# Performance work log

Measured on AMD Instinct MI355X. Metric: run time of the kernel, lower is better.

## Reference

```python
import jax, jax.numpy as jnp
import numpy as np

NUM_HEADS = 8
EMBED_DIM = 512
MAX_SEQ = 2048
HEAD_DIM = EMBED_DIM // NUM_HEADS
B, S = 2, 2048


def setup_inputs() -> dict:
    key = jax.random.key(0)
    ks = jax.random.split(key, 12)
    sd = 1.0 / np.sqrt(EMBED_DIM)
    return {
        "q_in": jax.random.normal(ks[0], (B, S, EMBED_DIM), jnp.float32),
        "k_in": jax.random.normal(ks[1], (B, S, EMBED_DIM), jnp.float32),
        "v_in": jax.random.normal(ks[2], (B, S, EMBED_DIM), jnp.float32),
        "Wq": jax.random.normal(ks[3], (EMBED_DIM, EMBED_DIM), jnp.float32) * sd,
        "bq": jnp.zeros((EMBED_DIM,), jnp.float32),
        "Wk": jax.random.normal(ks[4], (EMBED_DIM, EMBED_DIM), jnp.float32) * sd,
        "bk": jnp.zeros((EMBED_DIM,), jnp.float32),
        "Wv": jax.random.normal(ks[5], (EMBED_DIM, EMBED_DIM), jnp.float32) * sd,
        "bv": jnp.zeros((EMBED_DIM,), jnp.float32),
        "Wo": jax.random.normal(ks[6], (EMBED_DIM, EMBED_DIM), jnp.float32) * sd,
        "bo": jnp.zeros((EMBED_DIM,), jnp.float32),
        "rel_emb": jax.random.normal(ks[7], (MAX_SEQ, HEAD_DIM), jnp.float32) * sd,
    }


def _split_heads(x, W, b):
    # x: [B,S,E] -> [B,H,S,D]
    y = x @ W + b
    b_, s_ = y.shape[0], y.shape[1]
    return y.reshape(b_, s_, NUM_HEADS, HEAD_DIM).transpose(0, 2, 1, 3)


def _relative_scores(q, rel_emb):
    # q: [B,H,L,D]; rel_emb sliced to last L rows: [M,D] with M == L here
    L = q.shape[2]
    rel = rel_emb[max(0, MAX_SEQ - L):, :]
    M = rel.shape[0]
    scores = jnp.einsum('bhld,md->bhlm', q, rel)
    # mask = flip(tri(L,M), axis=-1): zero out future relative positions
    mask = jnp.flip(jnp.tri(L, M, dtype=jnp.float32), axis=1)
    scores = scores * mask
    # skew trick: pad one column on the left, reshape swapping last two dims, drop first row
    padded = jnp.pad(scores, ((0, 0), (0, 0), (0, 0), (1, 0)))  # [B,H,L,M+1]
    reshaped = padded.reshape(padded.shape[0], padded.shape[1], M + 1, L)
    skewed = reshaped[:, :, 1:, :]  # [B,H,M,L] == [B,H,L,L]
    return skewed


def reference(q_in, k_in, v_in, Wq, bq, Wk, bk, Wv, bv, Wo, bo, rel_emb):
    q = _split_heads(q_in, Wq, bq)  # [B,H,S,D]
    k = _split_heads(k_in, Wk, bk)
    v = _split_heads(v_in, Wv, bv)
    scores = jnp.einsum('bhqd,bhkd->bhqk', q, k)
    rel_scores = _relative_scores(q, rel_emb)
    logits = (scores + rel_scores) / jnp.sqrt(jnp.float32(HEAD_DIM))
    attn = jax.nn.softmax(logits, axis=-1)
    out = jnp.einsum('bhqk,bhkd->bhqd', attn, v)  # [B,H,S,D]
    merged = out.transpose(0, 2, 1, 3).reshape(out.shape[0], -1, EMBED_DIM)
    return merged @ Wo + bo, attn
```

## Files before the change

kernel.cpp:

```cpp
#include <hip/hip_runtime.h>


typedef __attribute__((ext_vector_type(4))) float f32x4;
typedef __attribute__((ext_vector_type(8))) short short8;

__device__ inline unsigned short f2bf(float x) {
    unsigned u = __float_as_uint(x);
    unsigned r = (u + 0x7fffu + ((u >> 16) & 1u)) >> 16;
    return (unsigned short)r;
}
__device__ inline float bf2f(unsigned short h) {
    return __uint_as_float(((unsigned)h) << 16);
}
__device__ inline int swz(int row, int bytecol) {
    return (row << 7) + (bytecol ^ ((row & 7) << 4));
}
__device__ inline void cvt4(float4 v, uint2& hi, uint2& lo) {
    unsigned short h0 = f2bf(v.x), h1 = f2bf(v.y), h2 = f2bf(v.z), h3 = f2bf(v.w);
    hi = make_uint2(((unsigned)h1 << 16) | h0, ((unsigned)h3 << 16) | h2);
    lo = make_uint2(((unsigned)f2bf(v.y - bf2f(h1)) << 16) | f2bf(v.x - bf2f(h0)),
                    ((unsigned)f2bf(v.w - bf2f(h3)) << 16) | f2bf(v.z - bf2f(h2)));
}
__device__ inline uint2 cvt4hi(float4 v) {
    return make_uint2(((unsigned)f2bf(v.y) << 16) | f2bf(v.x),
                      ((unsigned)f2bf(v.w) << 16) | f2bf(v.z));
}

__global__ __launch_bounds__(256) void wt_prep4(const float* __restrict__ W0,
                                                const float* __restrict__ W1,
                                                const float* __restrict__ W2,
                                                const float* __restrict__ W3,
                                                unsigned short* __restrict__ wt)
{
    __shared__ float Ls[32][33];
    const int t = threadIdx.x;
    const int z = blockIdx.z;
    const float* W = (z == 0) ? W0 : (z == 1) ? W1 : (z == 2) ? W2 : W3;
    unsigned short* WTh = wt + (size_t)(2 * z) * 262144;
    unsigned short* WTl = wt + (size_t)(2 * z + 1) * 262144;
    const int k0 = blockIdx.x << 5, n0 = blockIdx.y << 5;
#pragma unroll
    for (int i = 0; i < 4; ++i) {
        int idx = (i << 8) + t;
        int kk = idx >> 5, nn = idx & 31;
        Ls[kk][nn] = W[(size_t)(k0 + kk) * 512 + n0 + nn];
    }
    __syncthreads();
#pragma unroll
    for (int i = 0; i < 2; ++i) {
        int idx = (i << 8) + t;
        int nn = idx >> 4, kp = idx & 15;
        float f0 = Ls[2 * kp][nn], f1 = Ls[2 * kp + 1][nn];
        unsigned short h0 = f2bf(f0), h1 = f2bf(f1);
        size_t off = (size_t)(n0 + nn) * 512 + k0 + 2 * kp;
        *(unsigned*)&WTh[off] = ((unsigned)h1 << 16) | h0;
        *(unsigned*)&WTl[off] = ((unsigned)f2bf(f1 - bf2f(h1)) << 16) | f2bf(f0 - bf2f(h0));
    }
}

__global__ __launch_bounds__(256) void rel_prep(const float* __restrict__ rel,
                                                unsigned short* __restrict__ relh)
{
    int idx = (blockIdx.x * 256 + threadIdx.x) << 3;
    float4 a = *(const float4*)&rel[idx];
    float4 b = *(const float4*)&rel[idx + 4];
    uint4 o;
    o.x = ((unsigned)f2bf(a.y) << 16) | f2bf(a.x);
    o.y = ((unsigned)f2bf(a.w) << 16) | f2bf(a.z);
    o.z = ((unsigned)f2bf(b.y) << 16) | f2bf(b.x);
    o.w = ((unsigned)f2bf(b.w) << 16) | f2bf(b.z);
    *(uint4*)&relh[idx] = o;
}

__device__ __forceinline__ void gemm64_core(const float* __restrict__ A,
                                            const unsigned short* __restrict__ WTh,
                                            const unsigned short* __restrict__ WTl,
                                            int m0, int n0, char* smem, int t,
                                            f32x4 (&acc)[4])
{
    char* aH = smem;
    char* aL = smem + 8192;
    char* wH = smem + 16384;
    char* wL = smem + 24576;
    const int lane = t & 63, w = t >> 6;
    const int lr = lane & 15, kg = lane >> 4;

    for (int k0 = 0; k0 < 512; k0 += 64) {
        if (k0) __syncthreads();
#pragma unroll
        for (int i = 0; i < 4; ++i) {
            int idx = (i << 8) + t;
            int row = idx >> 4, c4 = idx & 15;
            float4 v = *(const float4*)&A[(size_t)(m0 + row) * 512 + k0 + (c4 << 2)];
            uint2 hi, lo; cvt4(v, hi, lo);
            int ph = swz(row, c4 << 3);
            *(uint2*)(aH + ph) = hi;
            *(uint2*)(aL + ph) = lo;
        }
#pragma unroll
        for (int i = 0; i < 4; ++i) {
            int idx = (i << 8) + t;
            int plane = idx >> 9, rem = idx & 511;
            int nn = rem >> 3, j8 = rem & 7;
            const unsigned short* src = plane ? WTl : WTh;
            uint4 vv = *(const uint4*)&src[(size_t)(n0 + nn) * 512 + k0 + (j8 << 3)];
            *(uint4*)((plane ? wL : wH) + swz(nn, j8 << 4)) = vv;
        }
        __syncthreads();
#pragma unroll
        for (int kk = 0; kk < 2; ++kk) {
            int bc = (kk << 6) + (kg << 4);
            int ar = (w << 4) + lr;
            short8 a_h = *(const short8*)(aH + swz(ar, bc));
            short8 a_l = *(const short8*)(aL + swz(ar, bc));
#pragma unroll
            for (int f = 0; f < 4; ++f) {
                short8 b_h = *(const short8*)(wH + swz((f << 4) + lr, bc));
                short8 b_l = *(const short8*)(wL + swz((f << 4) + lr, bc));
                acc[f] = __builtin_amdgcn_mfma_f32_16x16x32_bf16(a_h, b_h, acc[f], 0, 0, 0);
                acc[f] = __builtin_amdgcn_mfma_f32_16x16x32_bf16(a_l, b_h, acc[f], 0, 0, 0);
                acc[f] = __builtin_amdgcn_mfma_f32_16x16x32_bf16(a_h, b_l, acc[f], 0, 0, 0);
            }
        }
    }
}

__global__ __launch_bounds__(256) void gemm_qkv(
    const float* __restrict__ Aq, const float* __restrict__ Ak, const float* __restrict__ Av,
    const unsigned short* __restrict__ wt,
    const float* __restrict__ bq, const float* __restrict__ bk, const float* __restrict__ bv,
    unsigned short* __restrict__ qh, unsigned short* __restrict__ ql,
    unsigned short* __restrict__ kh, unsigned short* __restrict__ kl,
    unsigned short* __restrict__ vh, unsigned short* __restrict__ vl)
{
    __shared__ char smem[32768];
    const int t = threadIdx.x;
    const int z = blockIdx.z;
    const int n0 = blockIdx.x << 6;
    const int m0 = blockIdx.y << 6;
    const int lane = t & 63, w = t >> 6;
    const int lr = lane & 15, kg = lane >> 4;

    const float* A = (z == 0) ? Aq : (z == 1) ? Ak : Av;
    const float* bias = (z == 0) ? bq : (z == 1) ? bk : bv;
    const unsigned short* WTh = wt + (size_t)(2 * z) * 262144;
    const unsigned short* WTl = wt + (size_t)(2 * z + 1) * 262144;
    unsigned short* outH = (z == 0) ? qh : (z == 1) ? kh : vh;
    unsigned short* outL = (z == 0) ? ql : (z == 1) ? kl : vl;

    f32x4 acc[4];
#pragma unroll
    for (int f = 0; f < 4; ++f) acc[f] = {0.f, 0.f, 0.f, 0.f};

    gemm64_core(A, WTh, WTl, m0, n0, smem, t, acc);

    const int mbase = m0 + (w << 4) + (kg << 2);
    const int b = mbase >> 11, s = mbase & 2047;
    const int bidx = (b << 3) + (n0 >> 6);
#pragma unroll
    for (int f = 0; f < 4; ++f) {
        int d = (f << 4) + lr;
        float bv_ = bias[n0 + d];
        if (z < 2) {
#pragma unroll
            for (int e = 0; e < 4; ++e) {
                float val = acc[f][e] + bv_;
                unsigned short hh = f2bf(val);
                size_t off = ((size_t)bidx * 2048 + s + e) * 64 + d;
                outH[off] = hh;
                outL[off] = f2bf(val - bf2f(hh));
            }
        } else {
            unsigned short h[4], l[4];
#pragma unroll
            for (int e = 0; e < 4; ++e) {
                float val = acc[f][e] + bv_;
                h[e] = f2bf(val);
                l[e] = f2bf(val - bf2f(h[e]));
            }
            size_t off = ((size_t)bidx * 64 + d) * 2048 + s;
            *(uint2*)&outH[off] = make_uint2(((unsigned)h[1] << 16) | h[0],
                                             ((unsigned)h[3] << 16) | h[2]);
            *(uint2*)&outL[off] = make_uint2(((unsigned)l[1] << 16) | l[0],
                                             ((unsigned)l[3] << 16) | l[2]);
        }
    }
}

__global__ __launch_bounds__(256) void gemm_out(
    const float* __restrict__ pO,
    const unsigned short* __restrict__ WTh, const unsigned short* __restrict__ WTl,
    const float* __restrict__ bias, float* __restrict__ out0)
{
    __shared__ char smem[32768];
    char* aH = smem;
    char* aL = smem + 8192;
    char* wH = smem + 16384;
    char* wL = smem + 24576;
    const int t = threadIdx.x;
    const int n0 = blockIdx.x << 6;
    const int m0 = blockIdx.y << 6;
    const int lane = t & 63, w = t >> 6;
    const int lr = lane & 15, kg = lane >> 4;
    const int bq = m0 >> 11, s0 = m0 & 2047;

    f32x4 acc[4];
#pragma unroll
    for (int f = 0; f < 4; ++f) acc[f] = {0.f, 0.f, 0.f, 0.f};

    for (int k0 = 0; k0 < 512; k0 += 64) {
        if (k0) __syncthreads();
        const float* p0 = pO + ((size_t)((bq << 3) + (k0 >> 6)) * 2048 + s0) * 64;
#pragma unroll
        for (int i = 0; i < 2; ++i) {
            int idx = (i << 8) + t;
            int row = idx >> 3, j8 = idx & 7;
            size_t off = (size_t)row * 64 + (j8 << 3);
            float4 a0 = *(const float4*)&p0[off];
            float4 a1 = *(const float4*)&p0[off + 4];
            float4 b0 = *(const float4*)&p0[off + 2097152];
            float4 b1 = *(const float4*)&p0[off + 4 + 2097152];
            float4 v0 = make_float4(a0.x + b0.x, a0.y + b0.y, a0.z + b0.z, a0.w + b0.w);
            float4 v1 = make_float4(a1.x + b1.x, a1.y + b1.y, a1.z + b1.z, a1.w + b1.w);
            uint2 h0, l0, h1, l1;
            cvt4(v0, h0, l0);
            cvt4(v1, h1, l1);
            int ph = swz(row, j8 << 4);
            *(uint4*)(aH + ph) = make_uint4(h0.x, h0.y, h1.x, h1.y);
            *(uint4*)(aL + ph) = make_uint4(l0.x, l0.y, l1.x, l1.y);
        }
#pragma unroll
        for (int i = 0; i < 4; ++i) {
            int idx = (i << 8) + t;
            int plane = idx >> 9, rem = idx & 511;
            int nn = rem >> 3, j8 = rem & 7;
            const unsigned short* src = plane ? WTl : WTh;
            uint4 vv = *(const uint4*)&src[(size_t)(n0 + nn) * 512 + k0 + (j8 << 3)];
            *(uint4*)((plane ? wL : wH) + swz(nn, j8 << 4)) = vv;
        }
        __syncthreads();
#pragma unroll
        for (int kk = 0; kk < 2; ++kk) {
            int bc = (kk << 6) + (kg << 4);
            int ar = (w << 4) + lr;
            short8 a_h = *(const short8*)(aH + swz(ar, bc));
            short8 a_l = *(const short8*)(aL + swz(ar, bc));
#pragma unroll
            for (int f = 0; f < 4; ++f) {
                short8 b_h = *(const short8*)(wH + swz((f << 4) + lr, bc));
                short8 b_l = *(const short8*)(wL + swz((f << 4) + lr, bc));
                acc[f] = __builtin_amdgcn_mfma_f32_16x16x32_bf16(a_h, b_h, acc[f], 0, 0, 0);
                acc[f] = __builtin_amdgcn_mfma_f32_16x16x32_bf16(a_l, b_h, acc[f], 0, 0, 0);
                acc[f] = __builtin_amdgcn_mfma_f32_16x16x32_bf16(a_h, b_l, acc[f], 0, 0, 0);
            }
        }
    }

    const int mbase = m0 + (w << 4) + (kg << 2);
#pragma unroll
    for (int f = 0; f < 4; ++f) {
        int n = n0 + (f << 4) + lr;
        float bv = bias[n];
#pragma unroll
        for (int e = 0; e < 4; ++e)
            out0[(size_t)(mbase + e) * 512 + n] = acc[f][e] + bv;
    }
}

__global__ __launch_bounds__(512, 4) void logits_flash(
    const unsigned short* __restrict__ qh_g, const unsigned short* __restrict__ ql_g,
    const unsigned short* __restrict__ kh_g, const unsigned short* __restrict__ kl_g,
    const unsigned short* __restrict__ relh_g,
    float* __restrict__ attn, unsigned short* __restrict__ rawh,
    float* __restrict__ tilemax, int mode,
    float2* __restrict__ stats)
{
    __shared__ char smem[59136];
    char* kh = smem;
    char* kl = smem + 16384;
    char* bandP = smem + 32768;
    unsigned short* Pt = (unsigned short*)(smem + 32768);
    float* part_m = (float*)(smem + 58112);
    float* part_z = (float*)(smem + 58624);

    const int t = threadIdx.x;
    const int bh = blockIdx.y;
    int ib = blockIdx.x; if (bh & 8) ib = 31 - ib;
    const int i0 = ib << 6;
    const int lane = t & 63, w = t >> 6;
    const int wr = w >> 1, wc = w & 1;
    const int lr = lane & 15, kg = lane >> 4;
    const int irow = (wr << 4) + lr;

    const size_t qoff = ((size_t)bh * 2048 + i0 + irow) * 64;
    const short8 aH0 = *(const short8*)(qh_g + qoff + (kg << 3));
    const short8 aH1 = *(const short8*)(qh_g + qoff + 32 + (kg << 3));
    const short8 aL0 = *(const short8*)(ql_g + qoff + (kg << 3));
    const short8 aL1 = *(const short8*)(ql_g + qoff + 32 + (kg << 3));

    float rm = -3.0e38f, rz = 0.f;

    const unsigned short* khb = kh_g + (size_t)bh * 2048 * 64;
    const unsigned short* klb = kl_g + (size_t)bh * 2048 * 64;
    const size_t obase = ((size_t)bh * 2048 + i0) * 2048;

    for (int jt = 0; jt < 16; ++jt) {
        const int j0 = jt << 7;
        const bool anyRel = (j0 <= i0 + 63);
        const int m0 = 1984 - i0 + j0;
        __syncthreads();
        if (jt > 0 && t < 64) {
            float m1 = part_m[t], m2 = part_m[64 + t];
            float z1 = part_z[t], z2 = part_z[64 + t];
            float tm = fmaxf(m1, m2);
            float tz = z1 * __expf((m1 - tm) * 0.125f) + z2 * __expf((m2 - tm) * 0.125f);
            float mn = fmaxf(rm, tm);
            rz = rz * __expf((rm - mn) * 0.125f) + tz * __expf((tm - mn) * 0.125f);
            rm = mn;
        }
        {
            int rr = t >> 2, gp = (t & 3) << 1;
            const unsigned short* s0 = khb + (size_t)(j0 + rr) * 64 + (gp << 3);
            *(uint4*)(kh + swz(rr, gp << 4)) = *(const uint4*)s0;
            *(uint4*)(kh + swz(rr, (gp + 1) << 4)) = *(const uint4*)(s0 + 8);
            const unsigned short* s1 = klb + (size_t)(j0 + rr) * 64 + (gp << 3);
            *(uint4*)(kl + swz(rr, gp << 4)) = *(const uint4*)s1;
            *(uint4*)(kl + swz(rr, (gp + 1) << 4)) = *(const uint4*)(s1 + 8);
        }
        if (anyRel) {
#pragma unroll
            for (int i = 0; i < 3; ++i) {
                int idx = (i << 9) + t;
                int row = idx >> 3, g = idx & 7;
                int m = m0 + row; if (m > 2047) m = 2047;
                *(uint4*)(bandP + swz(row, g << 4)) = *(const uint4*)(relh_g + (size_t)m * 64 + (g << 3));
            }
        }
        __syncthreads();

        f32x4 acc[4];
#pragma unroll
        for (int cf = 0; cf < 4; ++cf) {
            int krow = (wc << 6) + (cf << 4) + lr;
            short8 bH0 = *(const short8*)(kh + swz(krow, kg << 4));
            short8 bH1 = *(const short8*)(kh + swz(krow, 64 + (kg << 4)));
            short8 bL0 = *(const short8*)(kl + swz(krow, kg << 4));
            short8 bL1 = *(const short8*)(kl + swz(krow, 64 + (kg << 4)));
            f32x4 c = {0.f, 0.f, 0.f, 0.f};
            c = __builtin_amdgcn_mfma_f32_16x16x32_bf16(bH0, aH0, c, 0, 0, 0);
            c = __builtin_amdgcn_mfma_f32_16x16x32_bf16(bH1, aH1, c, 0, 0, 0);
            c = __builtin_amdgcn_mfma_f32_16x16x32_bf16(bH0, aL0, c, 0, 0, 0);
            c = __builtin_amdgcn_mfma_f32_16x16x32_bf16(bH1, aL1, c, 0, 0, 0);
            c = __builtin_amdgcn_mfma_f32_16x16x32_bf16(bL0, aH0, c, 0, 0, 0);
            c = __builtin_amdgcn_mfma_f32_16x16x32_bf16(bL1, aH1, c, 0, 0, 0);
            acc[cf] = c;
        }
        if (anyRel) {
            f32x4 pr[6];
#pragma unroll
            for (int q = 0; q < 6; ++q) {
                int ff = (wc ? 6 : 0) + q;
                int brow = (ff << 4) + lr;
                short8 rb0 = *(const short8*)(bandP + swz(brow, kg << 4));
                short8 rb1 = *(const short8*)(bandP + swz(brow, 64 + (kg << 4)));
                f32x4 c = {0.f, 0.f, 0.f, 0.f};
                c = __builtin_amdgcn_mfma_f32_16x16x32_bf16(rb0, aH0, c, 0, 0, 0);
                c = __builtin_amdgcn_mfma_f32_16x16x32_bf16(rb1, aH1, c, 0, 0, 0);
                pr[q] = c;
            }
            __syncthreads();
#pragma unroll
            for (int q = 0; q < 6; ++q) {
                int ff = (wc ? 6 : 0) + q;
#pragma unroll
                for (int e = 0; e < 4; ++e)
                    Pt[((ff << 4) + (kg << 2) + e) * 66 + irow] = f2bf(pr[q][e]);
            }
            __syncthreads();
        }

        float rowmax = -3.0e38f;
#pragma unroll
        for (int cf = 0; cf < 4; ++cf) {
            int jl0 = (wc << 6) + (cf << 4) + (kg << 2);
            f32x4 a = acc[cf];
#pragma unroll
            for (int e = 0; e < 4; ++e) {
                int jl = jl0 + e;
                if (anyRel && (jl - irow) <= (i0 - j0))
                    a[e] += bf2f(Pt[(jl + 63 - irow) * 66 + irow]);
            }
            acc[cf] = a;
            rowmax = fmaxf(rowmax, fmaxf(fmaxf(a[0], a[1]), fmaxf(a[2], a[3])));
        }
        rowmax = fmaxf(rowmax, __shfl_xor(rowmax, 16, 64));
        rowmax = fmaxf(rowmax, __shfl_xor(rowmax, 32, 64));

        float zs = 0.f;
#pragma unroll
        for (int cf = 0; cf < 4; ++cf) {
            int jl0 = (wc << 6) + (cf << 4) + (kg << 2);
            f32x4 a = acc[cf];
            f32x4 u;
#pragma unroll
            for (int e = 0; e < 4; ++e) {
                u[e] = __expf((a[e] - rowmax) * 0.125f);
                zs += u[e];
            }
            size_t oidx = obase + (size_t)irow * 2048 + j0 + jl0;
            if (mode == 2) {
                *(uint2*)&rawh[oidx] = make_uint2(
                    (unsigned)f2bf(u[0]) | ((unsigned)f2bf(u[1]) << 16),
                    (unsigned)f2bf(u[2]) | ((unsigned)f2bf(u[3]) << 16));
            } else if (mode == 1) {
                *(uint2*)&rawh[oidx] = make_uint2(
                    (unsigned)f2bf(a[0]) | ((unsigned)f2bf(a[1]) << 16),
                    (unsigned)f2bf(a[2]) | ((unsigned)f2bf(a[3]) << 16));
            } else {
                *(float4*)&attn[oidx] = make_float4(a[0], a[1], a[2], a[3]);
            }
        }
        zs += __shfl_xor(zs, 16, 64);
        zs += __shfl_xor(zs, 32, 64);
        if (lane < 16) {
            part_m[(wc << 6) + irow] = rowmax;
            part_z[(wc << 6) + irow] = zs;
            if (mode == 2)
                tilemax[(size_t)((jt << 1) + wc) * 32768 + bh * 2048 + i0 + irow] = rowmax;
        }
    }
    __syncthreads();
    if (t < 64) {
        float m1 = part_m[t], m2 = part_m[64 + t];
        float z1 = part_z[t], z2 = part_z[64 + t];
        float tm = fmaxf(m1, m2);
        float tz = z1 * __expf((m1 - tm) * 0.125f) + z2 * __expf((m2 - tm) * 0.125f);
        float mn = fmaxf(rm, tm);
        rz = rz * __expf((rm - mn) * 0.125f) + tz * __expf((tm - mn) * 0.125f);
        rm = mn;
        stats[bh * 2048 + i0 + t] = make_float2(rm, 1.0f / rz);
    }
}

__global__ __launch_bounds__(256) void pv_mm(const float* __restrict__ attn,
                                             const unsigned short* __restrict__ rawh,
                                             const float* __restrict__ tilemax, int mode,
                                             const unsigned short* __restrict__ vTh,
                                             const unsigned short* __restrict__ vTl,
                                             const float2* __restrict__ stats,
                                             float* __restrict__ pO)
{
    __shared__ char smem[25088];
    char* pH = smem;
    char* vH = smem + 8192;
    char* vL = smem + 16384;
    float2* sm = (float2*)(smem + 24576);

    const int t = threadIdx.x;
    const int i0 = blockIdx.x << 6;
    const int bh = blockIdx.y;
    const int jc = blockIdx.z;
    const int jc0 = jc << 10;
    const int lane = t & 63, w = t >> 6;
    const int lr = lane & 15, kg = lane >> 4;

    const float* ab = attn + ((size_t)bh * 2048 + i0) * 2048;
    const unsigned short* rb = rawh + ((size_t)bh * 2048 + i0) * 2048;
    const unsigned short* vhb = vTh + (size_t)bh * 64 * 2048;
    const unsigned short* vlb = vTl + (size_t)bh * 64 * 2048;
    const int tmbase = bh * 2048 + i0;

    if (t < 64) sm[t] = stats[bh * 2048 + i0 + t];
    __syncthreads();

    f32x4 acc[4];
#pragma unroll
    for (int f = 0; f < 4; ++f) acc[f] = {0.f, 0.f, 0.f, 0.f};

    for (int j0 = jc0; j0 < jc0 + 1024; j0 += 64) {
        if (j0 != jc0) __syncthreads();
        const int half = j0 >> 6;
#pragma unroll
        for (int i = 0; i < 4; ++i) {
            int idx = (i << 8) + t;
            int row = idx >> 4, c4 = idx & 15;
            size_t go = (size_t)row * 2048 + j0 + (c4 << 2);
            float2 s2 = sm[row];
            float4 p;
            if (mode == 2) {
                uint2 rv = *(const uint2*)&rb[go];
                float corr = __expf((tilemax[(size_t)half * 32768 + tmbase + row] - s2.x) * 0.125f) * s2.y;
                p.x = bf2f((unsigned short)(rv.x & 0xffff)) * corr;
                p.y = bf2f((unsigned short)(rv.x >> 16)) * corr;
                p.z = bf2f((unsigned short)(rv.y & 0xffff)) * corr;
                p.w = bf2f((unsigned short)(rv.y >> 16)) * corr;
            } else {
                float4 x;
                if (mode == 1) {
                    uint2 rv = *(const uint2*)&rb[go];
                    x = make_float4(bf2f((unsigned short)(rv.x & 0xffff)),
                                    bf2f((unsigned short)(rv.x >> 16)),
                                    bf2f((unsigned short)(rv.y & 0xffff)),
                                    bf2f((unsigned short)(rv.y >> 16)));
                } else {
                    x = *(const float4*)&ab[go];
                }
                p.x = __expf((x.x - s2.x) * 0.125f) * s2.y;
                p.y = __expf((x.y - s2.x) * 0.125f) * s2.y;
                p.z = __expf((x.z - s2.x) * 0.125f) * s2.y;
                p.w = __expf((x.w - s2.x) * 0.125f) * s2.y;
            }
            *(uint2*)(pH + swz(row, c4 << 3)) = cvt4hi(p);
        }
#pragma unroll
        for (int i = 0; i < 4; ++i) {
            int idx = (i << 8) + t;
            int plane = idx >> 9, rem = idx & 511;
            int d = rem >> 3, g8 = rem & 7;
            const unsigned short* src = (plane ? vlb : vhb) + (size_t)d * 2048 + j0 + (g8 << 3);
            *(uint4*)((plane ? vL : vH) + swz(d, g8 << 4)) = *(const uint4*)src;
        }
        __syncthreads();
#pragma unroll
        for (int kk = 0; kk < 2; ++kk) {
            int bc = (kk << 6) + (kg << 4);
            int ar = (w << 4) + lr;
            short8 a_h = *(const short8*)(pH + swz(ar, bc));
#pragma unroll
            for (int f = 0; f < 4; ++f) {
                short8 b_h = *(const short8*)(vH + swz((f << 4) + lr, bc));
                short8 b_l = *(const short8*)(vL + swz((f << 4) + lr, bc));
                acc[f] = __builtin_amdgcn_mfma_f32_16x16x32_bf16(a_h, b_h, acc[f], 0, 0, 0);
                acc[f] = __builtin_amdgcn_mfma_f32_16x16x32_bf16(a_h, b_l, acc[f], 0, 0, 0);
            }
        }
    }
#pragma unroll
    for (int f = 0; f < 4; ++f) {
#pragma unroll
        for (int e = 0; e < 4; ++e) {
            int m = i0 + (w << 4) + (kg << 2) + e;
            pO[(size_t)jc * 2097152 + ((size_t)bh * 2048 + m) * 64 + (f << 4) + lr] = acc[f][e];
        }
    }
}

__global__ __launch_bounds__(256) void norm_stream(float* __restrict__ attn,
                                                   const unsigned short* __restrict__ rawh,
                                                   const float* __restrict__ tilemax, int mode,
                                                   const float2* __restrict__ stats)
{
    const int t = threadIdx.x;
    const int lane = t & 63, w = t >> 6;
    const int row = (blockIdx.x << 2) + w;
    const float2 s2 = stats[row];
    float* arow = attn + (size_t)row * 2048;
    const unsigned short* urow = rawh + (size_t)row * 2048;

#pragma unroll
    for (int c = 0; c < 8; ++c) {
        int col = (c << 8) + (lane << 2);
        float4 p;
        if (mode == 2) {
            uint2 rv = *(const uint2*)&urow[col];
            float corr = __expf((tilemax[(size_t)(col >> 6) * 32768 + row] - s2.x) * 0.125f) * s2.y;
            p.x = bf2f((unsigned short)(rv.x & 0xffff)) * corr;
            p.y = bf2f((unsigned short)(rv.x >> 16)) * corr;
            p.z = bf2f((unsigned short)(rv.y & 0xffff)) * corr;
            p.w = bf2f((unsigned short)(rv.y >> 16)) * corr;
        } else {
            float4 x;
            if (mode == 1) {
                uint2 rv = *(const uint2*)&urow[col];
                x = make_float4(bf2f((unsigned short)(rv.x & 0xffff)),
                                bf2f((unsigned short)(rv.x >> 16)),
                                bf2f((unsigned short)(rv.y & 0xffff)),
                                bf2f((unsigned short)(rv.y >> 16)));
            } else {
                x = *(const float4*)&arow[col];
            }
            p.x = __expf((x.x - s2.x) * 0.125f) * s2.y;
            p.y = __expf((x.y - s2.x) * 0.125f) * s2.y;
            p.z = __expf((x.z - s2.x) * 0.125f) * s2.y;
            p.w = __expf((x.w - s2.x) * 0.125f) * s2.y;
        }
        *(float4*)&arow[col] = p;
    }
}

extern "C" void kernel_launch(void* const* d_in, const int* in_sizes, int n_in,
                              void* d_out, int out_size, void* d_ws, size_t ws_size,
                              hipStream_t stream)
{
    const float* q_in = (const float*)d_in[0];
    const float* k_in = (const float*)d_in[1];
    const float* v_in = (const float*)d_in[2];
    const float* Wq   = (const float*)d_in[3];
    const float* bq   = (const float*)d_in[4];
    const float* Wk   = (const float*)d_in[5];
    const float* bk   = (const float*)d_in[6];
    const float* Wv   = (const float*)d_in[7];
    const float* bv   = (const float*)d_in[8];
    const float* Wo   = (const float*)d_in[9];
    const float* bo   = (const float*)d_in[10];
    const float* rel  = (const float*)d_in[11];

    float* out0 = (float*)d_out;
    float* attn = out0 + 2097152;

    float* ws = (float*)d_ws;
    unsigned short* qh = (unsigned short*)ws;
    unsigned short* ql = qh + 2097152;
    unsigned short* kh = (unsigned short*)(ws + 2097152);
    unsigned short* kl = kh + 2097152;
    unsigned short* vTh = (unsigned short*)(ws + 4194304);
    unsigned short* vTl = vTh + 2097152;
    unsigned short* wt = (unsigned short*)(ws + 6291456);
    unsigned short* relh = (unsigned short*)(ws + 7340032);
    float2* stats = (float2*)(ws + 7405568);
    unsigned short* rawh = (unsigned short*)(ws + 7471104);
    float* tilemax = ws + 41025536;
    float* pO = ws;

    const int mode = (ws_size >= 168296448ULL) ? 2
                   : (ws_size >= 164102144ULL) ? 1 : 0;

    wt_prep4<<<dim3(16, 16, 4), 256, 0, stream>>>(Wq, Wk, Wv, Wo, wt);
    rel_prep<<<64, 256, 0, stream>>>(rel, relh);

    gemm_qkv<<<dim3(8, 64, 3), 256, 0, stream>>>(q_in, k_in, v_in, wt,
                                                 bq, bk, bv,
                                                 qh, ql, kh, kl, vTh, vTl);

    logits_flash<<<dim3(32, 16), 512, 0, stream>>>(qh, ql, kh, kl, relh,
                                                   attn, rawh, tilemax, mode, stats);
    pv_mm<<<dim3(32, 16, 2), 256, 0, stream>>>(attn, rawh, tilemax, mode,
                                               vTh, vTl, stats, pO);
    gemm_out<<<dim3(8, 64), 256, 0, stream>>>(pO,
                                              wt + 6 * 262144, wt + 7 * 262144,
                                              bo, out0);
    norm_stream<<<8192, 256, 0, stream>>>(attn, rawh, tilemax, mode, stats);
}
```

Before: 325.3 us.

## Fuse normalization and PV matmul into logits kernel for bf16 raw mode

In mode 2, a new logits_fused kernel computes the raw exponentials and tile maxima, then, within the same block, rereads its own rows, applies the final per-tile correction, writes the normalized attention and multiplies by V to produce the per-head output. This removes the separate pv_mm and norm_stream launches and the split-K pO reduction, so gemm_out reads a single partial buffer. In exchange, each block serialises the PV phase after the logits phase, which lowers parallelism for the PV work (no split over j), and the block re-reads rawh from global memory, relying on a threadfence for visibility.

```diff
diff --git a/kernel.cpp b/kernel.cpp
--- a/kernel.cpp
+++ b/kernel.cpp
@@ -188,7 +188,7 @@
 }
 
 __global__ __launch_bounds__(256) void gemm_out(
-    const float* __restrict__ pO,
+    const float* __restrict__ pO, int single,
     const unsigned short* __restrict__ WTh, const unsigned short* __restrict__ WTl,
     const float* __restrict__ bias, float* __restrict__ out0)
 {
@@ -216,12 +216,14 @@
             int idx = (i << 8) + t;
             int row = idx >> 3, j8 = idx & 7;
             size_t off = (size_t)row * 64 + (j8 << 3);
-            float4 a0 = *(const float4*)&p0[off];
-            float4 a1 = *(const float4*)&p0[off + 4];
-            float4 b0 = *(const float4*)&p0[off + 2097152];
-            float4 b1 = *(const float4*)&p0[off + 4 + 2097152];
-            float4 v0 = make_float4(a0.x + b0.x, a0.y + b0.y, a0.z + b0.z, a0.w + b0.w);
-            float4 v1 = make_float4(a1.x + b1.x, a1.y + b1.y, a1.z + b1.z, a1.w + b1.w);
+            float4 v0 = *(const float4*)&p0[off];
+            float4 v1 = *(const float4*)&p0[off + 4];
+            if (!single) {
+                float4 b0 = *(const float4*)&p0[off + 2097152];
+                float4 b1 = *(const float4*)&p0[off + 4 + 2097152];
+                v0 = make_float4(v0.x + b0.x, v0.y + b0.y, v0.z + b0.z, v0.w + b0.w);
+                v1 = make_float4(v1.x + b1.x, v1.y + b1.y, v1.z + b1.z, v1.w + b1.w);
+            }
             uint2 h0, l0, h1, l1;
             cvt4(v0, h0, l0);
             cvt4(v1, h1, l1);
@@ -267,13 +269,14 @@
     }
 }
 
-__global__ __launch_bounds__(512, 4) void logits_flash(
+__global__ __launch_bounds__(512, 4) void logits_fused(
     const unsigned short* __restrict__ qh_g, const unsigned short* __restrict__ ql_g,
     const unsigned short* __restrict__ kh_g, const unsigned short* __restrict__ kl_g,
     const unsigned short* __restrict__ relh_g,
     float* __restrict__ attn, unsigned short* __restrict__ rawh,
-    float* __restrict__ tilemax, int mode,
-    float2* __restrict__ stats)
+    float* __restrict__ tilemax,
+    const unsigned short* __restrict__ vTh, const unsigned short* __restrict__ vTl,
+    float* __restrict__ pO)
 {
     __shared__ char smem[59136];
     char* kh = smem;
@@ -303,6 +306,7 @@
     const unsigned short* khb = kh_g + (size_t)bh * 2048 * 64;
     const unsigned short* klb = kl_g + (size_t)bh * 2048 * 64;
     const size_t obase = ((size_t)bh * 2048 + i0) * 2048;
+    const int tmbase = bh * 2048 + i0;
 
     for (int jt = 0; jt < 16; ++jt) {
         const int j0 = jt << 7;
@@ -408,11 +412,240 @@
                 zs += u[e];
             }
             size_t oidx = obase + (size_t)irow * 2048 + j0 + jl0;
-            if (mode == 2) {
-                *(uint2*)&rawh[oidx] = make_uint2(
-                    (unsigned)f2bf(u[0]) | ((unsigned)f2bf(u[1]) << 16),
-                    (unsigned)f2bf(u[2]) | ((unsigned)f2bf(u[3]) << 16));
-            } else if (mode == 1) {
+            *(uint2*)&rawh[oidx] = make_uint2(
+                (unsigned)f2bf(u[0]) | ((unsigned)f2bf(u[1]) << 16),
+                (unsigned)f2bf(u[2]) | ((unsigned)f2bf(u[3]) << 16));
+        }
+        zs += __shfl_xor(zs, 16, 64);
+        zs += __shfl_xor(zs, 32, 64);
+        if (lane < 16) {
+            part_m[(wc << 6) + irow] = rowmax;
+            part_z[(wc << 6) + irow] = zs;
+            tilemax[(size_t)((jt << 1) + wc) * 32768 + tmbase + irow] = rowmax;
+        }
+    }
+    __threadfence();
+    __syncthreads();
+    if (t < 64) {
+        float m1 = part_m[t], m2 = part_m[64 + t];
+        float z1 = part_z[t], z2 = part_z[64 + t];
+        float tm = fmaxf(m1, m2);
+        float tz = z1 * __expf((m1 - tm) * 0.125f) + z2 * __expf((m2 - tm) * 0.125f);
+        float mn = fmaxf(rm, tm);
+        rz = rz * __expf((rm - mn) * 0.125f) + tz * __expf((tm - mn) * 0.125f);
+        part_m[t] = mn;
+        part_z[t] = 1.0f / rz;
+    }
+    __syncthreads();
+
+    char* pU = smem;
+    char* vH = smem + 16384;
+    char* vL = smem + 24576;
+    const int rw0 = (w & 3) << 4;
+    const int dw0 = (w >> 2) << 5;
+    const unsigned short* rb = rawh + obase;
+    float* ab = attn + obase;
+    const unsigned short* vhb = vTh + (size_t)bh * 64 * 2048;
+    const unsigned short* vlb = vTl + (size_t)bh * 64 * 2048;
+
+    f32x4 oacc[2];
+    oacc[0] = {0.f, 0.f, 0.f, 0.f};
+    oacc[1] = {0.f, 0.f, 0.f, 0.f};
+
+    for (int j0 = 0; j0 < 2048; j0 += 64) {
+        if (j0) __syncthreads();
+        const int half = j0 >> 6;
+#pragma unroll
+        for (int i = 0; i < 2; ++i) {
+            int idx = (i << 9) + t;
+            int row = idx >> 4, c4 = idx & 15;
+            size_t go = (size_t)row * 2048 + j0 + (c4 << 2);
+            uint2 rv = *(const uint2*)&rb[go];
+            float corr = __expf((tilemax[(size_t)half * 32768 + tmbase + row] - part_m[row]) * 0.125f)
+                         * part_z[row];
+            float4 p;
+            p.x = bf2f((unsigned short)(rv.x & 0xffff)) * corr;
+            p.y = bf2f((unsigned short)(rv.x >> 16)) * corr;
+            p.z = bf2f((unsigned short)(rv.y & 0xffff)) * corr;
+            p.w = bf2f((unsigned short)(rv.y >> 16)) * corr;
+            *(float4*)&ab[go] = p;
+            *(uint2*)(pU + swz(row, c4 << 3)) = cvt4hi(p);
+        }
+#pragma unroll
+        for (int i = 0; i < 2; ++i) {
+            int idx = (i << 9) + t;
+            int plane = idx >> 9, rem = idx & 511;
+            int d = rem >> 3, g8 = rem & 7;
+            const unsigned short* src = (plane ? vlb : vhb) + (size_t)d * 2048 + j0 + (g8 << 3);
+            *(uint4*)((plane ? vL : vH) + swz(d, g8 << 4)) = *(const uint4*)src;
+        }
+        __syncthreads();
+#pragma unroll
+        for (int kk = 0; kk < 2; ++kk) {
+            int bc = (kk << 6) + (kg << 4);
+            short8 a_h = *(const short8*)(pU + swz(rw0 + lr, bc));
+#pragma unroll
+            for (int f = 0; f < 2; ++f) {
+                int vrow = dw0 + (f << 4) + lr;
+                short8 b_h = *(const short8*)(vH + swz(vrow, bc));
+                short8 b_l = *(const short8*)(vL + swz(vrow, bc));
+                oacc[f] = __builtin_amdgcn_mfma_f32_16x16x32_bf16(a_h, b_h, oacc[f], 0, 0, 0);
+                oacc[f] = __builtin_amdgcn_mfma_f32_16x16x32_bf16(a_h, b_l, oacc[f], 0, 0, 0);
+            }
+        }
+    }
+#pragma unroll
+    for (int f = 0; f < 2; ++f) {
+#pragma unroll
+        for (int e = 0; e < 4; ++e) {
+            int m = i0 + rw0 + (kg << 2) + e;
+            pO[((size_t)bh * 2048 + m) * 64 + dw0 + (f << 4) + lr] = oacc[f][e];
+        }
+    }
+}
+
+__global__ __launch_bounds__(512, 4) void logits_flash(
+    const unsigned short* __restrict__ qh_g, const unsigned short* __restrict__ ql_g,
+    const unsigned short* __restrict__ kh_g, const unsigned short* __restrict__ kl_g,
+    const unsigned short* __restrict__ relh_g,
+    float* __restrict__ attn, unsigned short* __restrict__ rawh,
+    float* __restrict__ tilemax, int mode,
+    float2* __restrict__ stats)
+{
+    __shared__ char smem[59136];
+    char* kh = smem;
+    char* kl = smem + 16384;
+    char* bandP = smem + 32768;
+    unsigned short* Pt = (unsigned short*)(smem + 32768);
+    float* part_m = (float*)(smem + 58112);
+    float* part_z = (float*)(smem + 58624);
+
+    const int t = threadIdx.x;
+    const int bh = blockIdx.y;
+    int ib = blockIdx.x; if (bh & 8) ib = 31 - ib;
+    const int i0 = ib << 6;
+    const int lane = t & 63, w = t >> 6;
+    const int wr = w >> 1, wc = w & 1;
+    const int lr = lane & 15, kg = lane >> 4;
+    const int irow = (wr << 4) + lr;
+
+    const size_t qoff = ((size_t)bh * 2048 + i0 + irow) * 64;
+    const short8 aH0 = *(const short8*)(qh_g + qoff + (kg << 3));
+    const short8 aH1 = *(const short8*)(qh_g + qoff + 32 + (kg << 3));
+    const short8 aL0 = *(const short8*)(ql_g + qoff + (kg << 3));
+    const short8 aL1 = *(const short8*)(ql_g + qoff + 32 + (kg << 3));
+
+    float rm = -3.0e38f, rz = 0.f;
+
+    const unsigned short* khb = kh_g + (size_t)bh * 2048 * 64;
+    const unsigned short* klb = kl_g + (size_t)bh * 2048 * 64;
+    const size_t obase = ((size_t)bh * 2048 + i0) * 2048;
+
+    for (int jt = 0; jt < 16; ++jt) {
+        const int j0 = jt << 7;
+        const bool anyRel = (j0 <= i0 + 63);
+        const int m0 = 1984 - i0 + j0;
+        __syncthreads();
+        if (jt > 0 && t < 64) {
+            float m1 = part_m[t], m2 = part_m[64 + t];
+            float z1 = part_z[t], z2 = part_z[64 + t];
+            float tm = fmaxf(m1, m2);
+            float tz = z1 * __expf((m1 - tm) * 0.125f) + z2 * __expf((m2 - tm) * 0.125f);
+            float mn = fmaxf(rm, tm);
+            rz = rz * __expf((rm - mn) * 0.125f) + tz * __expf((tm - mn) * 0.125f);
+            rm = mn;
+        }
+        {
+            int rr = t >> 2, gp = (t & 3) << 1;
+            const unsigned short* s0 = khb + (size_t)(j0 + rr) * 64 + (gp << 3);
+            *(uint4*)(kh + swz(rr, gp << 4)) = *(const uint4*)s0;
+            *(uint4*)(kh + swz(rr, (gp + 1) << 4)) = *(const uint4*)(s0 + 8);
+            const unsigned short* s1 = klb + (size_t)(j0 + rr) * 64 + (gp << 3);
+            *(uint4*)(kl + swz(rr, gp << 4)) = *(const uint4*)s1;
+            *(uint4*)(kl + swz(rr, (gp + 1) << 4)) = *(const uint4*)(s1 + 8);
+        }
+        if (anyRel) {
+#pragma unroll
+            for (int i = 0; i < 3; ++i) {
+                int idx = (i << 9) + t;
+                int row = idx >> 3, g = idx & 7;
+                int m = m0 + row; if (m > 2047) m = 2047;
+                *(uint4*)(bandP + swz(row, g << 4)) = *(const uint4*)(relh_g + (size_t)m * 64 + (g << 3));
+            }
+        }
+        __syncthreads();
+
+        f32x4 acc[4];
+#pragma unroll
+        for (int cf = 0; cf < 4; ++cf) {
+            int krow = (wc << 6) + (cf << 4) + lr;
+            short8 bH0 = *(const short8*)(kh + swz(krow, kg << 4));
+            short8 bH1 = *(const short8*)(kh + swz(krow, 64 + (kg << 4)));
+            short8 bL0 = *(const short8*)(kl + swz(krow, kg << 4));
+            short8 bL1 = *(const short8*)(kl + swz(krow, 64 + (kg << 4)));
+            f32x4 c = {0.f, 0.f, 0.f, 0.f};
+            c = __builtin_amdgcn_mfma_f32_16x16x32_bf16(bH0, aH0, c, 0, 0, 0);
+            c = __builtin_amdgcn_mfma_f32_16x16x32_bf16(bH1, aH1, c, 0, 0, 0);
+            c = __builtin_amdgcn_mfma_f32_16x16x32_bf16(bH0, aL0, c, 0, 0, 0);
+            c = __builtin_amdgcn_mfma_f32_16x16x32_bf16(bH1, aL1, c, 0, 0, 0);
+            c = __builtin_amdgcn_mfma_f32_16x16x32_bf16(bL0, aH0, c, 0, 0, 0);
+            c = __builtin_amdgcn_mfma_f32_16x16x32_bf16(bL1, aH1, c, 0, 0, 0);
+            acc[cf] = c;
+        }
+        if (anyRel) {
+            f32x4 pr[6];
+#pragma unroll
+            for (int q = 0; q < 6; ++q) {
+                int ff = (wc ? 6 : 0) + q;
+                int brow = (ff << 4) + lr;
+                short8 rb0 = *(const short8*)(bandP + swz(brow, kg << 4));
+                short8 rb1 = *(const short8*)(bandP + swz(brow, 64 + (kg << 4)));
+                f32x4 c = {0.f, 0.f, 0.f, 0.f};
+                c = __builtin_amdgcn_mfma_f32_16x16x32_bf16(rb0, aH0, c, 0, 0, 0);
+                c = __builtin_amdgcn_mfma_f32_16x16x32_bf16(rb1, aH1, c, 0, 0, 0);
+                pr[q] = c;
+            }
+            __syncthreads();
+#pragma unroll
+            for (int q = 0; q < 6; ++q) {
+                int ff = (wc ? 6 : 0) + q;
+#pragma unroll
+                for (int e = 0; e < 4; ++e)
+                    Pt[((ff << 4) + (kg << 2) + e) * 66 + irow] = f2bf(pr[q][e]);
+            }
+            __syncthreads();
+        }
+
+        float rowmax = -3.0e38f;
+#pragma unroll
+        for (int cf = 0; cf < 4; ++cf) {
+            int jl0 = (wc << 6) + (cf << 4) + (kg << 2);
+            f32x4 a = acc[cf];
+#pragma unroll
+            for (int e = 0; e < 4; ++e) {
+                int jl = jl0 + e;
+                if (anyRel && (jl - irow) <= (i0 - j0))
+                    a[e] += bf2f(Pt[(jl + 63 - irow) * 66 + irow]);
+            }
+            acc[cf] = a;
+            rowmax = fmaxf(rowmax, fmaxf(fmaxf(a[0], a[1]), fmaxf(a[2], a[3])));
+        }
+        rowmax = fmaxf(rowmax, __shfl_xor(rowmax, 16, 64));
+        rowmax = fmaxf(rowmax, __shfl_xor(rowmax, 32, 64));
+
+        float zs = 0.f;
+#pragma unroll
+        for (int cf = 0; cf < 4; ++cf) {
+            int jl0 = (wc << 6) + (cf << 4) + (kg << 2);
+            f32x4 a = acc[cf];
+            f32x4 u;
+#pragma unroll
+            for (int e = 0; e < 4; ++e) {
+                u[e] = __expf((a[e] - rowmax) * 0.125f);
+                zs += u[e];
+            }
+            size_t oidx = obase + (size_t)irow * 2048 + j0 + jl0;
+            if (mode == 1) {
                 *(uint2*)&rawh[oidx] = make_uint2(
                     (unsigned)f2bf(a[0]) | ((unsigned)f2bf(a[1]) << 16),
                     (unsigned)f2bf(a[2]) | ((unsigned)f2bf(a[3]) << 16));
@@ -425,8 +658,6 @@
         if (lane < 16) {
             part_m[(wc << 6) + irow] = rowmax;
             part_z[(wc << 6) + irow] = zs;
-            if (mode == 2)
-                tilemax[(size_t)((jt << 1) + wc) * 32768 + bh * 2048 + i0 + irow] = rowmax;
         }
     }
     __syncthreads();
@@ -444,7 +675,7 @@
 
 __global__ __launch_bounds__(256) void pv_mm(const float* __restrict__ attn,
                                              const unsigned short* __restrict__ rawh,
-                                             const float* __restrict__ tilemax, int mode,
+                                             int mode,
                                              const unsigned short* __restrict__ vTh,
                                              const unsigned short* __restrict__ vTl,
                                              const float2* __restrict__ stats,
@@ -468,7 +699,6 @@
     const unsigned short* rb = rawh + ((size_t)bh * 2048 + i0) * 2048;
     const unsigned short* vhb = vTh + (size_t)bh * 64 * 2048;
     const unsigned short* vlb = vTl + (size_t)bh * 64 * 2048;
-    const int tmbase = bh * 2048 + i0;
 
     if (t < 64) sm[t] = stats[bh * 2048 + i0 + t];
     __syncthreads();
@@ -479,37 +709,27 @@
 
     for (int j0 = jc0; j0 < jc0 + 1024; j0 += 64) {
         if (j0 != jc0) __syncthreads();
-        const int half = j0 >> 6;
 #pragma unroll
         for (int i = 0; i < 4; ++i) {
             int idx = (i << 8) + t;
             int row = idx >> 4, c4 = idx & 15;
             size_t go = (size_t)row * 2048 + j0 + (c4 << 2);
             float2 s2 = sm[row];
+            float4 x;
+            if (mode == 1) {
+                uint2 rv = *(const uint2*)&rb[go];
+                x = make_float4(bf2f((unsigned short)(rv.x & 0xffff)),
+                                bf2f((unsigned short)(rv.x >> 16)),
+                                bf2f((unsigned short)(rv.y & 0xffff)),
+                                bf2f((unsigned short)(rv.y >> 16)));
+            } else {
+                x = *(const float4*)&ab[go];
+            }
             float4 p;
-            if (mode == 2) {
-                uint2 rv = *(const uint2*)&rb[go];
-                float corr = __expf((tilemax[(size_t)half * 32768 + tmbase + row] - s2.x) * 0.125f) * s2.y;
-                p.x = bf2f((unsigned short)(rv.x & 0xffff)) * corr;
-                p.y = bf2f((unsigned short)(rv.x >> 16)) * corr;
-                p.z = bf2f((unsigned short)(rv.y & 0xffff)) * corr;
-                p.w = bf2f((unsigned short)(rv.y >> 16)) * corr;
-            } else {
-                float4 x;
-                if (mode == 1) {
-                    uint2 rv = *(const uint2*)&rb[go];
-                    x = make_float4(bf2f((unsigned short)(rv.x & 0xffff)),
-                                    bf2f((unsigned short)(rv.x >> 16)),
-                                    bf2f((unsigned short)(rv.y & 0xffff)),
-                                    bf2f((unsigned short)(rv.y >> 16)));
-                } else {
-                    x = *(const float4*)&ab[go];
-                }
-                p.x = __expf((x.x - s2.x) * 0.125f) * s2.y;
-                p.y = __expf((x.y - s2.x) * 0.125f) * s2.y;
-                p.z = __expf((x.z - s2.x) * 0.125f) * s2.y;
-                p.w = __expf((x.w - s2.x) * 0.125f) * s2.y;
-            }
+            p.x = __expf((x.x - s2.x) * 0.125f) * s2.y;
+            p.y = __expf((x.y - s2.x) * 0.125f) * s2.y;
+            p.z = __expf((x.z - s2.x) * 0.125f) * s2.y;
+            p.w = __expf((x.w - s2.x) * 0.125f) * s2.y;
             *(uint2*)(pH + swz(row, c4 << 3)) = cvt4hi(p);
         }
 #pragma unroll
@@ -547,7 +767,7 @@
 
 __global__ __launch_bounds__(256) void norm_stream(float* __restrict__ attn,
                                                    const unsigned short* __restrict__ rawh,
-                                                   const float* __restrict__ tilemax, int mode,
+                                                   int mode,
                                                    const float2* __restrict__ stats)
 {
     const int t = threadIdx.x;
@@ -560,30 +780,21 @@
 #pragma unroll
     for (int c = 0; c < 8; ++c) {
         int col = (c << 8) + (lane << 2);
+        float4 x;
+        if (mode == 1) {
+            uint2 rv = *(const uint2*)&urow[col];
+            x = make_float4(bf2f((unsigned short)(rv.x & 0xffff)),
+                            bf2f((unsigned short)(rv.x >> 16)),
+                            bf2f((unsigned short)(rv.y & 0xffff)),
+                            bf2f((unsigned short)(rv.y >> 16)));
+        } else {
+            x = *(const float4*)&arow[col];
+        }
         float4 p;
-        if (mode == 2) {
-            uint2 rv = *(const uint2*)&urow[col];
-            float corr = __expf((tilemax[(size_t)(col >> 6) * 32768 + row] - s2.x) * 0.125f) * s2.y;
-            p.x = bf2f((unsigned short)(rv.x & 0xffff)) * corr;
-            p.y = bf2f((unsigned short)(rv.x >> 16)) * corr;
-            p.z = bf2f((unsigned short)(rv.y & 0xffff)) * corr;
-            p.w = bf2f((unsigned short)(rv.y >> 16)) * corr;
-        } else {
-            float4 x;
-            if (mode == 1) {
-                uint2 rv = *(const uint2*)&urow[col];
-                x = make_float4(bf2f((unsigned short)(rv.x & 0xffff)),
-                                bf2f((unsigned short)(rv.x >> 16)),
-                                bf2f((unsigned short)(rv.y & 0xffff)),
-                                bf2f((unsigned short)(rv.y >> 16)));
-            } else {
-                x = *(const float4*)&arow[col];
-            }
-            p.x = __expf((x.x - s2.x) * 0.125f) * s2.y;
-            p.y = __expf((x.y - s2.x) * 0.125f) * s2.y;
-            p.z = __expf((x.z - s2.x) * 0.125f) * s2.y;
-            p.w = __expf((x.w - s2.x) * 0.125f) * s2.y;
-        }
+        p.x = __expf((x.x - s2.x) * 0.125f) * s2.y;
+        p.y = __expf((x.y - s2.x) * 0.125f) * s2.y;
+        p.z = __expf((x.z - s2.x) * 0.125f) * s2.y;
+        p.w = __expf((x.w - s2.x) * 0.125f) * s2.y;
         *(float4*)&arow[col] = p;
     }
 }
@@ -632,12 +843,21 @@
                                                  bq, bk, bv,
                                                  qh, ql, kh, kl, vTh, vTl);
 
-    logits_flash<<<dim3(32, 16), 512, 0, stream>>>(qh, ql, kh, kl, relh,
-                                                   attn, rawh, tilemax, mode, stats);
-    pv_mm<<<dim3(32, 16, 2), 256, 0, stream>>>(attn, rawh, tilemax, mode,
-                                               vTh, vTl, stats, pO);
-    gemm_out<<<dim3(8, 64), 256, 0, stream>>>(pO,
-                                              wt + 6 * 262144, wt + 7 * 262144,
-                                              bo, out0);
-    norm_stream<<<8192, 256, 0, stream>>>(attn, rawh, tilemax, mode, stats);
-}
+    if (mode == 2) {
+        logits_fused<<<dim3(32, 16), 512, 0, stream>>>(qh, ql, kh, kl, relh,
+                                                       attn, rawh, tilemax,
+                                                       vTh, vTl, pO);
+        gemm_out<<<dim3(8, 64), 256, 0, stream>>>(pO, 1,
+                                                  wt + 6 * 262144, wt + 7 * 262144,
+                                                  bo, out0);
+    } else {
+        logits_flash<<<dim3(32, 16), 512, 0, stream>>>(qh, ql, kh, kl, relh,
+                                                       attn, rawh, tilemax, mode, stats);
+        pv_mm<<<dim3(32, 16, 2), 256, 0, stream>>>(attn, rawh, mode,
+                                                   vTh, vTl, stats, pO);
+        gemm_out<<<dim3(8, 64), 256, 0, stream>>>(pO, 0,
+                                                  wt + 6 * 262144, wt + 7 * 262144,
+                                                  bo, out0);
+        norm_stream<<<8192, 256, 0, stream>>>(attn, rawh, mode, stats);
+    }
+}
```

After: 512.3 us. 1.57x slower.
